# Optimization experiments

Measured on AMD Instinct MI355X. Metric: run time of the kernel, lower is better.

Reference implementation:

```python
import jax, jax.numpy as jnp
import numpy as np

N, E, D, H = 50000, 800000, 64, 64  # nodes, edges, feat dim, hidden dim
EPS = 1e-3  # Keras BatchNormalization default epsilon

def bn(x, g, b, mu, v):
    # inference-mode batch norm with moving statistics
    return (x - mu) * jax.lax.rsqrt(v + EPS) * g + b

def gelu(x):
    return jax.nn.gelu(x, approximate=False)  # tf.nn.gelu default is exact

def setup_inputs() -> dict:
    key = jax.random.key(0)
    ks = jax.random.split(key, 24)
    r = lambda i, shape, s=1.0: (jax.random.normal(ks[i], shape, jnp.float32) * s)
    inp = {
        "node_feats": r(0, (N, D)),
        "edge_feats": r(1, (E, D)),
        "src": jax.random.randint(ks[2], (E,), 0, N, jnp.int32),
        "dst": jax.random.randint(ks[3], (E,), 0, N, jnp.int32),
        # message MLP (BN -> Dense(gelu)) x2, input D
        "m_g1": 1.0 + 0.1 * r(4, (D,)), "m_b1": 0.1 * r(5, (D,)),
        "m_mu1": 0.1 * r(6, (D,)), "m_v1": jnp.ones((D,), jnp.float32),
        "m_W1": r(7, (D, H), 1.0 / np.sqrt(D)), "m_c1": jnp.zeros((H,), jnp.float32),
        "m_g2": 1.0 + 0.1 * r(8, (H,)), "m_b2": 0.1 * r(9, (H,)),
        "m_mu2": 0.1 * r(10, (H,)), "m_v2": jnp.ones((H,), jnp.float32),
        "m_W2": r(11, (H, H), 1.0 / np.sqrt(H)), "m_c2": jnp.zeros((H,), jnp.float32),
        # edge transformer MLP (Dense(gelu)) x2, input D
        "e_W1": r(12, (D, H), 1.0 / np.sqrt(D)), "e_c1": jnp.zeros((H,), jnp.float32),
        "e_W2": r(13, (H, H), 1.0 / np.sqrt(H)), "e_c2": jnp.zeros((H,), jnp.float32),
        # update MLP (BN -> Dense(gelu)) x2, input D+H (concat combination)
        "u_g1": 1.0 + 0.1 * r(14, (D + H,)), "u_b1": 0.1 * r(15, (D + H,)),
        "u_mu1": 0.1 * r(16, (D + H,)), "u_v1": jnp.ones((D + H,), jnp.float32),
        "u_W1": r(17, (D + H, H), 1.0 / np.sqrt(D + H)), "u_c1": jnp.zeros((H,), jnp.float32),
        "u_g2": 1.0 + 0.1 * r(18, (H,)), "u_b2": 0.1 * r(19, (H,)),
        "u_mu2": 0.1 * r(20, (H,)), "u_v2": jnp.ones((H,), jnp.float32),
        "u_W2": r(21, (H, H), 1.0 / np.sqrt(H)), "u_c2": jnp.zeros((H,), jnp.float32),
    }
    return inp

def reference(node_feats, edge_feats,
              m_g1, m_b1, m_mu1, m_v1, m_W1, m_c1,
              m_g2, m_b2, m_mu2, m_v2, m_W2, m_c2,
              e_W1, e_c1, e_W2, e_c2,
              u_g1, u_b1, u_mu1, u_v1, u_W1, u_c1,
              u_g2, u_b2, u_mu2, u_v2, u_W2, u_c2,
              src, dst):
    # gather neighbour representations: [E, D]
    nbr = node_feats[dst]
    # base message MLP: (BN -> Dropout(identity at inference) -> Dense gelu) x2
    h = gelu(bn(nbr, m_g1, m_b1, m_mu1, m_v1) @ m_W1 + m_c1)
    msg = gelu(bn(h, m_g2, m_b2, m_mu2, m_v2) @ m_W2 + m_c2)
    # edge transformer: Dense(gelu) x2, gates the messages elementwise
    er = gelu(edge_feats @ e_W1 + e_c1)
    er = gelu(er @ e_W2 + e_c2)
    msg = msg * er  # [E, H]
    # unsorted_segment_mean over source node indices (empty segments -> 0)
    s = jax.ops.segment_sum(msg, src, num_segments=N)
    cnt = jax.ops.segment_sum(jnp.ones((E, 1), msg.dtype), src, num_segments=N)
    agg = s / jnp.maximum(cnt, 1.0)  # [N, H]
    # combine ('concat') and update MLP
    hcat = jnp.concatenate([node_feats, agg], axis=-1)  # [N, D+H]
    h = gelu(bn(hcat, u_g1, u_b1, u_mu1, u_v1) @ u_W1 + u_c1)
    out = gelu(bn(h, u_g2, u_b2, u_mu2, u_v2) @ u_W2 + u_c2)
    return out  # [N, H]
```

## Files before the change

kernel.cpp:

```cpp
#include <hip/hip_runtime.h>
#include <hip/hip_bf16.h>

#define NN 50000
#define NE 800000

typedef __bf16 bf16_t;
typedef bf16_t bf16x8 __attribute__((ext_vector_type(8)));
typedef float f32x4 __attribute__((ext_vector_type(4)));

__device__ __forceinline__ float gelu_f(float x) {
    float v = x * fmaf(x * x, 0.07135481627f, 1.595769122f);
    float e = __expf(-v);
    return x * __builtin_amdgcn_rcpf(1.0f + e);
}

__device__ void fold_frag(int K, const float* W, const float* g, const float* b,
                          const float* mu, const float* v, const float* c,
                          bf16_t* Wf, float* cb, int tid, float* part) {
    const int n = tid & 63, kc = tid >> 6;
    const int nt = n >> 4, lrow = n & 15, nkc = K >> 5;
    const int kq = K >> 2, k0 = kc * kq, k1 = k0 + kq;
    float acc = 0.f;
    for (int k = k0; k < k1; ++k) {
        float w = W[k * 64 + n];
        float s = 1.0f, o = 0.0f;
        if (g) {
            s = g[k] * __frsqrt_rn(v[k] + 1e-3f);
            o = b[k] - mu[k] * s;
        }
        int idx = ((nt * nkc + (k >> 5)) * 64 + ((k >> 3) & 3) * 16 + lrow) * 8 + (k & 7);
        Wf[idx] = (bf16_t)(w * s);
        acc += o * w;
    }
    part[kc * 64 + n] = acc;
    __syncthreads();
    if (kc == 0) cb[n] = c[n] + part[n] + part[64 + n] + part[128 + n] + part[192 + n];
}

__global__ void fold_kernel(
    const float* mg1, const float* mb1, const float* mmu1, const float* mv1,
    const float* mW1, const float* mc1,
    const float* mg2, const float* mb2, const float* mmu2, const float* mv2,
    const float* mW2, const float* mc2,
    const float* eW1, const float* ec1, const float* eW2, const float* ec2,
    const float* ug1, const float* ub1, const float* umu1, const float* uv1,
    const float* uW1, const float* uc1,
    const float* ug2, const float* ub2, const float* umu2, const float* uv2,
    const float* uW2, const float* uc2,
    bf16_t* wcat, bf16_t* uW1f, bf16_t* uW2f,
    float* cm1, float* cm2, float* ce1, float* ce2, float* cu1, float* cu2)
{
    __shared__ float part[256];
    int t = threadIdx.x;
    switch (blockIdx.x) {
        case 0: fold_frag(64,  mW1, mg1, mb1, mmu1, mv1, mc1, wcat,         cm1, t, part); break;
        case 1: fold_frag(64,  mW2, mg2, mb2, mmu2, mv2, mc2, wcat + 4096,  cm2, t, part); break;
        case 2: fold_frag(64,  eW1, nullptr, nullptr, nullptr, nullptr, ec1, wcat + 8192,  ce1, t, part); break;
        case 3: fold_frag(64,  eW2, nullptr, nullptr, nullptr, nullptr, ec2, wcat + 12288, ce2, t, part); break;
        case 4: fold_frag(128, uW1, ug1, ub1, umu1, uv1, uc1, uW1f, cu1, t, part); break;
        case 5: fold_frag(64,  uW2, ug2, ub2, umu2, uv2, uc2, uW2f, cu2, t, part); break;
    }
}

__global__ void hist_kernel(const int* __restrict__ src, int* __restrict__ cnt) {
    int e = blockIdx.x * 256 + threadIdx.x;
    if (e < NE) atomicAdd(&cnt[src[e]], 1);
}

__global__ void scanA_kernel(const int* __restrict__ cnt, int* __restrict__ part,
                             int* __restrict__ btot) {
    __shared__ int s[256];
    int tid = threadIdx.x;
    int i = blockIdx.x * 256 + tid;
    int v = (i < NN) ? cnt[i] : 0;
    s[tid] = v;
    __syncthreads();
    #pragma unroll
    for (int off = 1; off < 256; off <<= 1) {
        int t = (tid >= off) ? s[tid - off] : 0;
        __syncthreads();
        s[tid] += t;
        __syncthreads();
    }
    if (i < NN) part[i] = s[tid] - v;
    if (tid == 255) btot[blockIdx.x] = s[255];
}

__global__ void scanB_kernel(int* __restrict__ btot, int nblk) {
    __shared__ int s[256];
    int tid = threadIdx.x;
    int v = (tid < nblk) ? btot[tid] : 0;
    s[tid] = v;
    __syncthreads();
    #pragma unroll
    for (int off = 1; off < 256; off <<= 1) {
        int t = (tid >= off) ? s[tid - off] : 0;
        __syncthreads();
        s[tid] += t;
        __syncthreads();
    }
    if (tid < nblk) btot[tid] = s[tid] - v;
}

__global__ void scanC_kernel(const int* __restrict__ part, const int* __restrict__ btot,
                             int* __restrict__ woff) {
    int i = blockIdx.x * 256 + threadIdx.x;
    if (i < NN) woff[i] = part[i] + btot[i >> 8];
}

__device__ __forceinline__ void mk_frag_hilo(const float* row, int quad,
        bf16x8& hi0, bf16x8& lo0, bf16x8& hi1, bf16x8& lo1)
{
    #pragma unroll
    for (int j = 0; j < 8; ++j) {
        float x0 = row[quad * 8 + j];
        float x1 = row[32 + quad * 8 + j];
        bf16_t h0 = (bf16_t)x0, h1 = (bf16_t)x1;
        hi0[j] = h0; lo0[j] = (bf16_t)(x0 - (float)h0);
        hi1[j] = h1; lo1[j] = (bf16_t)(x1 - (float)h1);
    }
}

__device__ __forceinline__ bf16x8 ldb(const bf16_t* wf, int slot, int lane) {
    return *(const bf16x8*)(wf + (slot * 64 + lane) * 8);
}

__device__ __forceinline__ void gemm64_hilo(const bf16_t* wf, int m,
        bf16x8 h0, bf16x8 l0, bf16x8 h1, bf16x8 l1, f32x4 (&acc)[4], int lane)
{
    #pragma unroll
    for (int nt = 0; nt < 4; ++nt) {
        bf16x8 b0 = ldb(wf, m * 8 + nt * 2 + 0, lane);
        bf16x8 b1 = ldb(wf, m * 8 + nt * 2 + 1, lane);
        f32x4 c = {0.f, 0.f, 0.f, 0.f};
        c = __builtin_amdgcn_mfma_f32_16x16x32_bf16(h0, b0, c, 0, 0, 0);
        c = __builtin_amdgcn_mfma_f32_16x16x32_bf16(l0, b0, c, 0, 0, 0);
        c = __builtin_amdgcn_mfma_f32_16x16x32_bf16(h1, b1, c, 0, 0, 0);
        c = __builtin_amdgcn_mfma_f32_16x16x32_bf16(l1, b1, c, 0, 0, 0);
        acc[nt] = c;
    }
}

__device__ __forceinline__ void gemm64(const bf16_t* wf, int m,
        bf16x8 a0, bf16x8 a1, f32x4 (&acc)[4], int lane)
{
    #pragma unroll
    for (int nt = 0; nt < 4; ++nt) {
        bf16x8 b0 = ldb(wf, m * 8 + nt * 2 + 0, lane);
        bf16x8 b1 = ldb(wf, m * 8 + nt * 2 + 1, lane);
        f32x4 c = {0.f, 0.f, 0.f, 0.f};
        c = __builtin_amdgcn_mfma_f32_16x16x32_bf16(a0, b0, c, 0, 0, 0);
        c = __builtin_amdgcn_mfma_f32_16x16x32_bf16(a1, b1, c, 0, 0, 0);
        acc[nt] = c;
    }
}

__device__ __forceinline__ void epi_to_frag(const f32x4 (&acc)[4], const float* bias,
        bf16_t* h, int lrow, int quad)
{
    #pragma unroll
    for (int nt = 0; nt < 4; ++nt) {
        float bb = bias[nt * 16 + lrow];
        #pragma unroll
        for (int r = 0; r < 4; ++r)
            h[((nt * 2 + (lrow >> 3)) * 16 + quad * 4 + r) * 8 + (lrow & 7)] =
                (bf16_t)gelu_f(acc[nt][r] + bb);
    }
}

__global__ __launch_bounds__(256) void node_msg_kernel(
    const float* __restrict__ node_feats, const bf16_t* __restrict__ wcat,
    const float* __restrict__ cm1, const float* __restrict__ cm2,
    bf16_t* __restrict__ msg)
{
    __shared__ bf16_t wf[8192];
    __shared__ bf16_t hf[4][1024];

    const int tid  = threadIdx.x;
    const int wave = tid >> 6;
    const int lane = tid & 63;
    const int quad = lane >> 4;
    const int lrow = lane & 15;

    #pragma unroll
    for (int i = 0; i < 4; ++i) {
        int chunk = tid + i * 256;
        *(bf16x8*)(wf + chunk * 8) = *(const bf16x8*)(wcat + chunk * 8);
    }
    __syncthreads();

    const int nbase = blockIdx.x * 64 + wave * 16;
    int arow = nbase + lrow;
    arow = arow < NN ? arow : NN - 1;

    f32x4 acc[4];
    {
        const float* nrow = node_feats + (size_t)arow * 64;
        bf16x8 h0, l0, h1, l1;
        mk_frag_hilo(nrow, quad, h0, l0, h1, l1);
        gemm64_hilo(wf, 0, h0, l0, h1, l1, acc, lane);
        epi_to_frag(acc, cm1, hf[wave], lrow, quad);
    }
    bf16x8 a0 = *(const bf16x8*)(hf[wave] + lane * 8);
    bf16x8 a1 = *(const bf16x8*)(hf[wave] + (lane + 64) * 8);
    gemm64(wf, 1, a0, a1, acc, lane);

    #pragma unroll
    for (int nt = 0; nt < 4; ++nt) {
        float bb = cm2[nt * 16 + lrow];
        #pragma unroll
        for (int r = 0; r < 4; ++r) {
            int row = nbase + quad * 4 + r;
            if (row < NN)
                msg[(size_t)row * 64 + nt * 16 + lrow] = (bf16_t)gelu_f(acc[nt][r] + bb);
        }
    }
}

__global__ __launch_bounds__(256) void edge_kernel(
    const float* __restrict__ edge_feats,
    const int* __restrict__ src, const int* __restrict__ dst,
    const bf16_t* __restrict__ wcat,
    const float* __restrict__ ce1, const float* __restrict__ ce2,
    const bf16_t* __restrict__ msg,
    float* __restrict__ s_acc, int* __restrict__ woff,
    bf16_t* __restrict__ buf, int use_csr)
{
    __shared__ bf16_t wf[8192];
    __shared__ bf16_t hf[4][1024];
    __shared__ bf16_t sme[4][1024];

    const int tid  = threadIdx.x;
    const int wave = tid >> 6;
    const int lane = tid & 63;
    const int quad = lane >> 4;
    const int lrow = lane & 15;

    #pragma unroll
    for (int i = 0; i < 4; ++i) {
        int chunk = tid + i * 256;
        *(bf16x8*)(wf + chunk * 8) = *(const bf16x8*)(wcat + 8192 + chunk * 8);
    }
    __syncthreads();

    const int ebase = blockIdx.x * 64 + wave * 16;
    bf16_t* h  = hf[wave];
    bf16_t* sm = sme[wave];
    const int r0 = lane >> 3;
    const int c0 = lane & 7;
    const int r1 = 8 + r0;
    const int b0 = r0 * 64 + ((c0 * 8) ^ (((r0 >> 2) & 3) << 4));
    const int b1 = r1 * 64 + ((c0 * 8) ^ (((r1 >> 2) & 3) << 4));

    int dA = dst[ebase + r0];
    int dB = dst[ebase + r1];
    bf16x8 mA = *(const bf16x8*)(msg + (size_t)dA * 64 + c0 * 8);
    bf16x8 mB = *(const bf16x8*)(msg + (size_t)dB * 64 + c0 * 8);
    int pe_l = 0;
    if (use_csr && lane < 16) pe_l = atomicAdd(&woff[src[ebase + lane]], 1);

    f32x4 acc[4];
    {
        const float* efr = edge_feats + (size_t)(ebase + lrow) * 64;
        bf16x8 h0_, l0_, h1_, l1_;
        mk_frag_hilo(efr, quad, h0_, l0_, h1_, l1_);
        gemm64_hilo(wf, 0, h0_, l0_, h1_, l1_, acc, lane);
        epi_to_frag(acc, ce1, h, lrow, quad);
    }

    *(bf16x8*)(sm + b0) = mA;
    *(bf16x8*)(sm + b1) = mB;
    __builtin_amdgcn_wave_barrier();

    bf16x8 a0 = *(const bf16x8*)(h + lane * 8);
    bf16x8 a1 = *(const bf16x8*)(h + (lane + 64) * 8);
    gemm64(wf, 1, a0, a1, acc, lane);
    __builtin_amdgcn_wave_barrier();

    if (use_csr) {
        #pragma unroll
        for (int nt = 0; nt < 4; ++nt) {
            float bb = ce2[nt * 16 + lrow];
            #pragma unroll
            for (int r = 0; r < 4; ++r) {
                int e = quad * 4 + r;
                int ci = e * 64 + ((nt * 16 + lrow) ^ (((e >> 2) & 3) << 4));
                float er = gelu_f(acc[nt][r] + bb);
                sm[ci] = (bf16_t)(er * (float)sm[ci]);
            }
        }
        __builtin_amdgcn_wave_barrier();
        int peA = __shfl(pe_l, r0);
        int peB = __shfl(pe_l, r1);
        bf16x8 gA = *(const bf16x8*)(sm + b0);
        bf16x8 gB = *(const bf16x8*)(sm + b1);
        *(bf16x8*)(buf + (size_t)peA * 64 + c0 * 8) = gA;
        *(bf16x8*)(buf + (size_t)peB * 64 + c0 * 8) = gB;
    } else {
        #pragma unroll
        for (int nt = 0; nt < 4; ++nt) {
            float bb = ce2[nt * 16 + lrow];
            #pragma unroll
            for (int r = 0; r < 4; ++r) {
                int e = quad * 4 + r;
                int ci = e * 64 + ((nt * 16 + lrow) ^ (((e >> 2) & 3) << 4));
                float er = gelu_f(acc[nt][r] + bb);
                unsafeAtomicAdd(&s_acc[(size_t)src[ebase + e] * 64 + nt * 16 + lrow],
                                er * (float)sm[ci]);
            }
        }
    }
}

__global__ __launch_bounds__(256) void agg_kernel(
    const bf16_t* __restrict__ buf, const int* __restrict__ woff,
    const int* __restrict__ cnt, float* __restrict__ agg)
{
    const int wave = threadIdx.x >> 6;
    const int lane = threadIdx.x & 63;
    const int n = blockIdx.x * 4 + wave;
    const int deg = cnt[n];
    const int end = woff[n];
    const int start = end - deg;

    float s0 = 0.f, s1 = 0.f, s2 = 0.f, s3 = 0.f;
    const bf16_t* p = buf + (size_t)start * 64 + lane;
    int j = start;
    for (; j + 4 <= end; j += 4) {
        s0 += (float)p[0];
        s1 += (float)p[64];
        s2 += (float)p[128];
        s3 += (float)p[192];
        p += 256;
    }
    for (; j < end; ++j) { s0 += (float)p[0]; p += 64; }

    float r = (deg > 0) ? (s0 + s1 + s2 + s3) * __builtin_amdgcn_rcpf((float)deg) : 0.f;
    agg[(size_t)n * 64 + lane] = r;
}

__global__ __launch_bounds__(256) void update_kernel(
    const float* __restrict__ node_feats,
    const float* __restrict__ aggv, const int* __restrict__ cnt,
    const bf16_t* __restrict__ uW1f, const float* __restrict__ cu1,
    const bf16_t* __restrict__ uW2f, const float* __restrict__ cu2,
    float* __restrict__ out)
{
    __shared__ bf16_t w1f[8192];
    __shared__ bf16_t w2f[4096];
    __shared__ bf16_t hf[4][1024];

    const int tid  = threadIdx.x;
    const int wave = tid >> 6;
    const int lane = tid & 63;
    const int quad = lane >> 4;
    const int lrow = lane & 15;

    #pragma unroll
    for (int i = 0; i < 4; ++i) {
        int chunk = tid + i * 256;
        *(bf16x8*)(w1f + chunk * 8) = *(const bf16x8*)(uW1f + chunk * 8);
    }
    #pragma unroll
    for (int i = 0; i < 2; ++i) {
        int chunk = tid + i * 256;
        *(bf16x8*)(w2f + chunk * 8) = *(const bf16x8*)(uW2f + chunk * 8);
    }
    __syncthreads();

    const int nbase = blockIdx.x * 64 + wave * 16;
    int arow = nbase + lrow;
    arow = arow < NN ? arow : NN - 1;

    const float* nf   = node_feats + (size_t)arow * 64;
    const float* srow = aggv + (size_t)arow * 64;
    float inv = cnt ? 1.0f / fmaxf((float)cnt[arow], 1.0f) : 1.0f;

    bf16x8 ah[4], al[4];
    #pragma unroll
    for (int j = 0; j < 8; ++j) {
        float x0 = nf[quad * 8 + j];
        float x1 = nf[32 + quad * 8 + j];
        float x2 = srow[quad * 8 + j] * inv;
        float x3 = srow[32 + quad * 8 + j] * inv;
        bf16_t h0 = (bf16_t)x0, h1 = (bf16_t)x1, h2 = (bf16_t)x2, h3 = (bf16_t)x3;
        ah[0][j] = h0; al[0][j] = (bf16_t)(x0 - (float)h0);
        ah[1][j] = h1; al[1][j] = (bf16_t)(x1 - (float)h1);
        ah[2][j] = h2; al[2][j] = (bf16_t)(x2 - (float)h2);
        ah[3][j] = h3; al[3][j] = (bf16_t)(x3 - (float)h3);
    }

    f32x4 acc[4];
    #pragma unroll
    for (int nt = 0; nt < 4; ++nt) {
        f32x4 c = {0.f, 0.f, 0.f, 0.f};
        #pragma unroll
        for (int kk = 0; kk < 4; ++kk) {
            bf16x8 b = *(const bf16x8*)(w1f + ((nt * 4 + kk) * 64 + lane) * 8);
            c = __builtin_amdgcn_mfma_f32_16x16x32_bf16(ah[kk], b, c, 0, 0, 0);
            c = __builtin_amdgcn_mfma_f32_16x16x32_bf16(al[kk], b, c, 0, 0, 0);
        }
        acc[nt] = c;
    }
    bf16_t* hb = hf[wave];
    epi_to_frag(acc, cu1, hb, lrow, quad);

    bf16x8 ha0 = *(const bf16x8*)(hb + lane * 8);
    bf16x8 ha1 = *(const bf16x8*)(hb + (lane + 64) * 8);
    gemm64(w2f, 0, ha0, ha1, acc, lane);

    #pragma unroll
    for (int nt = 0; nt < 4; ++nt) {
        int col = nt * 16 + lrow;
        float bb = cu2[col];
        #pragma unroll
        for (int r = 0; r < 4; ++r) {
            int row = nbase + quad * 4 + r;
            if (row < NN)
                out[(size_t)row * 64 + col] = gelu_f(acc[nt][r] + bb);
        }
    }
}

extern "C" void kernel_launch(void* const* d_in, const int* in_sizes, int n_in,
                              void* d_out, int out_size, void* d_ws, size_t ws_size,
                              hipStream_t stream) {
    const float* node_feats = (const float*)d_in[0];
    const float* edge_feats = (const float*)d_in[1];
    const int*   src        = (const int*)d_in[2];
    const int*   dst        = (const int*)d_in[3];

    char* ws = (char*)d_ws;
    const bool csr = ws_size >= (size_t)116500000;

    size_t off = 0;
    bf16_t* buf = nullptr; float* agg = nullptr; bf16_t* msg = nullptr;
    float* s_acc = nullptr; int* cnt = nullptr; int* woff = nullptr;
    int* part = nullptr; int* btot = nullptr;

    if (csr) {
        buf = (bf16_t*)(ws + off); off += (size_t)NE * 128;
        char* aggbase = ws + off;
        agg = (float*)aggbase;     off += (size_t)NN * 256;
        msg = (bf16_t*)(aggbase + (size_t)NE * 4);
        cnt  = (int*)(ws + off); off += (size_t)NN * 4;
        woff = (int*)(ws + off); off += (size_t)NN * 4;
        part = (int*)(ws + off); off += (size_t)NN * 4;
        btot = (int*)(ws + off); off += 1024;
    } else {
        s_acc = (float*)(ws + off);  off += (size_t)NN * 256;
        cnt   = (int*)(ws + off);    off += (size_t)NN * 4;
        msg   = (bf16_t*)(ws + off); off += (size_t)NN * 128;
    }
    bf16_t* wcat = (bf16_t*)(ws + off); off += 32768;
    bf16_t* uW1f = (bf16_t*)(ws + off); off += 16384;
    bf16_t* uW2f = (bf16_t*)(ws + off); off += 8192;
    float* cm1 = (float*)(ws + off); off += 256;
    float* cm2 = (float*)(ws + off); off += 256;
    float* ce1 = (float*)(ws + off); off += 256;
    float* ce2 = (float*)(ws + off); off += 256;
    float* cu1 = (float*)(ws + off); off += 256;
    float* cu2 = (float*)(ws + off); off += 256;

    if (csr) {
        hipMemsetAsync(cnt, 0, (size_t)NN * 4, stream);
    } else {
        hipMemsetAsync(s_acc, 0, (size_t)NN * 256 + (size_t)NN * 4, stream);
    }

    fold_kernel<<<6, 256, 0, stream>>>(
        (const float*)d_in[4],  (const float*)d_in[5],  (const float*)d_in[6],  (const float*)d_in[7],
        (const float*)d_in[8],  (const float*)d_in[9],
        (const float*)d_in[10], (const float*)d_in[11], (const float*)d_in[12], (const float*)d_in[13],
        (const float*)d_in[14], (const float*)d_in[15],
        (const float*)d_in[16], (const float*)d_in[17], (const float*)d_in[18], (const float*)d_in[19],
        (const float*)d_in[20], (const float*)d_in[21], (const float*)d_in[22], (const float*)d_in[23],
        (const float*)d_in[24], (const float*)d_in[25],
        (const float*)d_in[26], (const float*)d_in[27], (const float*)d_in[28], (const float*)d_in[29],
        (const float*)d_in[30], (const float*)d_in[31],
        wcat, uW1f, uW2f, cm1, cm2, ce1, ce2, cu1, cu2);

    node_msg_kernel<<<(NN + 63) / 64, 256, 0, stream>>>(node_feats, wcat, cm1, cm2, msg);

    hist_kernel<<<(NE + 255) / 256, 256, 0, stream>>>(src, cnt);

    if (csr) {
        const int NBLK = (NN + 255) / 256;
        scanA_kernel<<<NBLK, 256, 0, stream>>>(cnt, part, btot);
        scanB_kernel<<<1, 256, 0, stream>>>(btot, NBLK);
        scanC_kernel<<<NBLK, 256, 0, stream>>>(part, btot, woff);
    }

    edge_kernel<<<NE / 64, 256, 0, stream>>>(
        edge_feats, src, dst, wcat, ce1, ce2, msg, s_acc, woff, buf, csr ? 1 : 0);

    if (csr) {
        agg_kernel<<<NN / 4, 256, 0, stream>>>(buf, woff, cnt, agg);
        update_kernel<<<(NN + 63) / 64, 256, 0, stream>>>(
            node_feats, agg, nullptr, uW1f, cu1, uW2f, cu2, (float*)d_out);
    } else {
        update_kernel<<<(NN + 63) / 64, 256, 0, stream>>>(
            node_feats, s_acc, cnt, uW1f, cu1, uW2f, cu2, (float*)d_out);
    }
}
```

Baseline: 484.2 us.

## Sort edges by source and reduce runs in-wave before atomic scatter

Replaces the two-path design (a CSR buffer of gated messages followed by a separate aggregation kernel, or per-element atomics) with one path. A fill kernel builds a source-sorted edge permutation, and the edge kernel processes edges in that order. Each wave sums consecutive edges that share a source node and issues one float atomic per run per feature. This removes the 100MB bf16 message buffer write and readback and the agg kernel. The cost is an extra permutation kernel, indirect (non-coalesced) reads of edge_feats rows, and nondeterministic float atomic order.

```diff
diff --git a/kernel.cpp b/kernel.cpp
--- a/kernel.cpp
+++ b/kernel.cpp
@@ -108,6 +108,15 @@
     if (i < NN) woff[i] = part[i] + btot[i >> 8];
 }
 
+__global__ void fill_kernel(const int* __restrict__ src, int* __restrict__ woff,
+                            int* __restrict__ eidx) {
+    int e = blockIdx.x * 256 + threadIdx.x;
+    if (e < NE) {
+        int p = atomicAdd(&woff[src[e]], 1);
+        eidx[p] = e;
+    }
+}
+
 __device__ __forceinline__ void mk_frag_hilo(const float* row, int quad,
         bf16x8& hi0, bf16x8& lo0, bf16x8& hi1, bf16x8& lo1)
 {
@@ -220,15 +229,16 @@
 __global__ __launch_bounds__(256) void edge_kernel(
     const float* __restrict__ edge_feats,
     const int* __restrict__ src, const int* __restrict__ dst,
+    const int* __restrict__ eidx,
     const bf16_t* __restrict__ wcat,
     const float* __restrict__ ce1, const float* __restrict__ ce2,
     const bf16_t* __restrict__ msg,
-    float* __restrict__ s_acc, int* __restrict__ woff,
-    bf16_t* __restrict__ buf, int use_csr)
+    float* __restrict__ s_acc)
 {
     __shared__ bf16_t wf[8192];
     __shared__ bf16_t hf[4][1024];
     __shared__ bf16_t sme[4][1024];
+    __shared__ int    nds[4][16];
 
     const int tid  = threadIdx.x;
     const int wave = tid >> 6;
@@ -243,25 +253,30 @@
     }
     __syncthreads();
 
-    const int ebase = blockIdx.x * 64 + wave * 16;
+    const int sbase = blockIdx.x * 64 + wave * 16;
     bf16_t* h  = hf[wave];
     bf16_t* sm = sme[wave];
+    int*    nd = nds[wave];
+
+    int e_lrow = eidx[sbase + lrow];
+    if (lane < 16) nd[lane] = src[e_lrow];
+
     const int r0 = lane >> 3;
     const int c0 = lane & 7;
     const int r1 = 8 + r0;
     const int b0 = r0 * 64 + ((c0 * 8) ^ (((r0 >> 2) & 3) << 4));
     const int b1 = r1 * 64 + ((c0 * 8) ^ (((r1 >> 2) & 3) << 4));
 
-    int dA = dst[ebase + r0];
-    int dB = dst[ebase + r1];
+    int eA = __shfl(e_lrow, r0);
+    int eB = __shfl(e_lrow, r1);
+    int dA = dst[eA];
+    int dB = dst[eB];
     bf16x8 mA = *(const bf16x8*)(msg + (size_t)dA * 64 + c0 * 8);
     bf16x8 mB = *(const bf16x8*)(msg + (size_t)dB * 64 + c0 * 8);
-    int pe_l = 0;
-    if (use_csr && lane < 16) pe_l = atomicAdd(&woff[src[ebase + lane]], 1);
 
     f32x4 acc[4];
     {
-        const float* efr = edge_feats + (size_t)(ebase + lrow) * 64;
+        const float* efr = edge_feats + (size_t)e_lrow * 64;
         bf16x8 h0_, l0_, h1_, l1_;
         mk_frag_hilo(efr, quad, h0_, l0_, h1_, l1_);
         gemm64_hilo(wf, 0, h0_, l0_, h1_, l1_, acc, lane);
@@ -277,66 +292,31 @@
     gemm64(wf, 1, a0, a1, acc, lane);
     __builtin_amdgcn_wave_barrier();
 
-    if (use_csr) {
+    #pragma unroll
+    for (int nt = 0; nt < 4; ++nt) {
+        float bb = ce2[nt * 16 + lrow];
         #pragma unroll
-        for (int nt = 0; nt < 4; ++nt) {
-            float bb = ce2[nt * 16 + lrow];
-            #pragma unroll
-            for (int r = 0; r < 4; ++r) {
-                int e = quad * 4 + r;
-                int ci = e * 64 + ((nt * 16 + lrow) ^ (((e >> 2) & 3) << 4));
-                float er = gelu_f(acc[nt][r] + bb);
-                sm[ci] = (bf16_t)(er * (float)sm[ci]);
-            }
-        }
-        __builtin_amdgcn_wave_barrier();
-        int peA = __shfl(pe_l, r0);
-        int peB = __shfl(pe_l, r1);
-        bf16x8 gA = *(const bf16x8*)(sm + b0);
-        bf16x8 gB = *(const bf16x8*)(sm + b1);
-        *(bf16x8*)(buf + (size_t)peA * 64 + c0 * 8) = gA;
-        *(bf16x8*)(buf + (size_t)peB * 64 + c0 * 8) = gB;
-    } else {
-        #pragma unroll
-        for (int nt = 0; nt < 4; ++nt) {
-            float bb = ce2[nt * 16 + lrow];
-            #pragma unroll
-            for (int r = 0; r < 4; ++r) {
-                int e = quad * 4 + r;
-                int ci = e * 64 + ((nt * 16 + lrow) ^ (((e >> 2) & 3) << 4));
-                float er = gelu_f(acc[nt][r] + bb);
-                unsafeAtomicAdd(&s_acc[(size_t)src[ebase + e] * 64 + nt * 16 + lrow],
-                                er * (float)sm[ci]);
-            }
-        }
-    }
-}
-
-__global__ __launch_bounds__(256) void agg_kernel(
-    const bf16_t* __restrict__ buf, const int* __restrict__ woff,
-    const int* __restrict__ cnt, float* __restrict__ agg)
-{
-    const int wave = threadIdx.x >> 6;
-    const int lane = threadIdx.x & 63;
-    const int n = blockIdx.x * 4 + wave;
-    const int deg = cnt[n];
-    const int end = woff[n];
-    const int start = end - deg;
-
-    float s0 = 0.f, s1 = 0.f, s2 = 0.f, s3 = 0.f;
-    const bf16_t* p = buf + (size_t)start * 64 + lane;
-    int j = start;
-    for (; j + 4 <= end; j += 4) {
-        s0 += (float)p[0];
-        s1 += (float)p[64];
-        s2 += (float)p[128];
-        s3 += (float)p[192];
-        p += 256;
-    }
-    for (; j < end; ++j) { s0 += (float)p[0]; p += 64; }
-
-    float r = (deg > 0) ? (s0 + s1 + s2 + s3) * __builtin_amdgcn_rcpf((float)deg) : 0.f;
-    agg[(size_t)n * 64 + lane] = r;
+        for (int r = 0; r < 4; ++r) {
+            int e = quad * 4 + r;
+            int ci = e * 64 + ((nt * 16 + lrow) ^ (((e >> 2) & 3) << 4));
+            float er = gelu_f(acc[nt][r] + bb);
+            sm[ci] = (bf16_t)(er * (float)sm[ci]);
+        }
+    }
+    __builtin_amdgcn_wave_barrier();
+
+    float run = 0.f;
+    int cur = nd[0];
+    #pragma unroll
+    for (int s = 0; s < 16; ++s) {
+        int n_s = nd[s];
+        if (n_s != cur) {
+            unsafeAtomicAdd(&s_acc[(size_t)cur * 64 + lane], run);
+            run = 0.f; cur = n_s;
+        }
+        run += (float)sm[s * 64 + (lane ^ (((s >> 2) & 3) << 4))];
+    }
+    unsafeAtomicAdd(&s_acc[(size_t)cur * 64 + lane], run);
 }
 
 __global__ __launch_bounds__(256) void update_kernel(
@@ -374,7 +354,7 @@
 
     const float* nf   = node_feats + (size_t)arow * 64;
     const float* srow = aggv + (size_t)arow * 64;
-    float inv = cnt ? 1.0f / fmaxf((float)cnt[arow], 1.0f) : 1.0f;
+    float inv = 1.0f / fmaxf((float)cnt[arow], 1.0f);
 
     bf16x8 ah[4], al[4];
     #pragma unroll
@@ -431,27 +411,14 @@
     const int*   dst        = (const int*)d_in[3];
 
     char* ws = (char*)d_ws;
-    const bool csr = ws_size >= (size_t)116500000;
-
     size_t off = 0;
-    bf16_t* buf = nullptr; float* agg = nullptr; bf16_t* msg = nullptr;
-    float* s_acc = nullptr; int* cnt = nullptr; int* woff = nullptr;
-    int* part = nullptr; int* btot = nullptr;
-
-    if (csr) {
-        buf = (bf16_t*)(ws + off); off += (size_t)NE * 128;
-        char* aggbase = ws + off;
-        agg = (float*)aggbase;     off += (size_t)NN * 256;
-        msg = (bf16_t*)(aggbase + (size_t)NE * 4);
-        cnt  = (int*)(ws + off); off += (size_t)NN * 4;
-        woff = (int*)(ws + off); off += (size_t)NN * 4;
-        part = (int*)(ws + off); off += (size_t)NN * 4;
-        btot = (int*)(ws + off); off += 1024;
-    } else {
-        s_acc = (float*)(ws + off);  off += (size_t)NN * 256;
-        cnt   = (int*)(ws + off);    off += (size_t)NN * 4;
-        msg   = (bf16_t*)(ws + off); off += (size_t)NN * 128;
-    }
+    float* s_acc = (float*)(ws + off);  off += (size_t)NN * 256;
+    int*   cnt   = (int*)(ws + off);    off += (size_t)NN * 4;
+    int*   woff  = (int*)(ws + off);    off += (size_t)NN * 4;
+    int*   part  = (int*)(ws + off);    off += (size_t)NN * 4;
+    int*   btot  = (int*)(ws + off);    off += 1024;
+    int*   eidx  = (int*)(ws + off);    off += (size_t)NE * 4;
+    bf16_t* msg  = (bf16_t*)(ws + off); off += (size_t)NN * 128;
     bf16_t* wcat = (bf16_t*)(ws + off); off += 32768;
     bf16_t* uW1f = (bf16_t*)(ws + off); off += 16384;
     bf16_t* uW2f = (bf16_t*)(ws + off); off += 8192;
@@ -462,11 +429,7 @@
     float* cu1 = (float*)(ws + off); off += 256;
     float* cu2 = (float*)(ws + off); off += 256;
 
-    if (csr) {
-        hipMemsetAsync(cnt, 0, (size_t)NN * 4, stream);
-    } else {
-        hipMemsetAsync(s_acc, 0, (size_t)NN * 256 + (size_t)NN * 4, stream);
-    }
+    hipMemsetAsync(s_acc, 0, (size_t)NN * 256 + (size_t)NN * 4, stream);
 
     fold_kernel<<<6, 256, 0, stream>>>(
         (const float*)d_in[4],  (const float*)d_in[5],  (const float*)d_in[6],  (const float*)d_in[7],
@@ -484,22 +447,15 @@
 
     hist_kernel<<<(NE + 255) / 256, 256, 0, stream>>>(src, cnt);
 
-    if (csr) {
-        const int NBLK = (NN + 255) / 256;
-        scanA_kernel<<<NBLK, 256, 0, stream>>>(cnt, part, btot);
-        scanB_kernel<<<1, 256, 0, stream>>>(btot, NBLK);
-        scanC_kernel<<<NBLK, 256, 0, stream>>>(part, btot, woff);
-    }
+    const int NBLK = (NN + 255) / 256;
+    scanA_kernel<<<NBLK, 256, 0, stream>>>(cnt, part, btot);
+    scanB_kernel<<<1, 256, 0, stream>>>(btot, NBLK);
+    scanC_kernel<<<NBLK, 256, 0, stream>>>(part, btot, woff);
+    fill_kernel<<<(NE + 255) / 256, 256, 0, stream>>>(src, woff, eidx);
 
     edge_kernel<<<NE / 64, 256, 0, stream>>>(
-        edge_feats, src, dst, wcat, ce1, ce2, msg, s_acc, woff, buf, csr ? 1 : 0);
-
-    if (csr) {
-        agg_kernel<<<NN / 4, 256, 0, stream>>>(buf, woff, cnt, agg);
-        update_kernel<<<(NN + 63) / 64, 256, 0, stream>>>(
-            node_feats, agg, nullptr, uW1f, cu1, uW2f, cu2, (float*)d_out);
-    } else {
-        update_kernel<<<(NN + 63) / 64, 256, 0, stream>>>(
-            node_feats, s_acc, cnt, uW1f, cu1, uW2f, cu2, (float*)d_out);
-    }
-}
+        edge_feats, src, dst, eidx, wcat, ce1, ce2, msg, s_acc);
+
+    update_kernel<<<(NN + 63) / 64, 256, 0, stream>>>(
+        node_feats, s_acc, cnt, uW1f, cu1, uW2f, cu2, (float*)d_out);
+}
```

Result: slower. 522.1 us (+7.8%).
